# Kernel optimization log

Hardware: AMD Instinct MI355X
Metric: run time of the kernel (lower is better)

## Reference

```python
import jax, jax.numpy as jnp
import numpy as np
from jax import lax

IMG_H, IMG_W = 800.0, 800.0
REG_WEIGHTS = (10.0, 10.0, 5.0, 5.0)
SCORE_THRESH = 0.05
NMS_THRESH = 0.5
NUM_DETECTIONS = 100
MIN_SIZE = 1.0
BBOX_XFORM_CLIP = float(np.log(1000.0 / 16.0))


def setup_inputs() -> dict:
    key = jax.random.key(0)
    k1, k2, k3, k4 = jax.random.split(key, 4)
    N, C = 1000, 81
    class_logit = jax.random.normal(k1, (N, C), dtype=jnp.float32) * 2.0
    box_regression = jax.random.normal(k2, (N, C * 4), dtype=jnp.float32)
    # proposals: valid (x1,y1,x2,y2) boxes inside the 800x800 image
    ctr = jax.random.uniform(k3, (N, 2), dtype=jnp.float32) * 800.0
    wh = jax.random.uniform(k4, (N, 2), dtype=jnp.float32) * 200.0 + 8.0
    x1y1 = jnp.clip(ctr - 0.5 * wh, 0.0, 800.0)
    x2y2 = jnp.clip(ctr + 0.5 * wh, 0.0, 800.0)
    proposal = jnp.concatenate([x1y1, x2y2], axis=1)
    return dict(class_logit=class_logit, box_regression=box_regression, proposal=proposal)


def decode_boxes(deltas, boxes):
    # deltas: [..., 4] (dx,dy,dw,dh); boxes: [..., 4] (x1,y1,x2,y2)
    wx, wy, ww, wh = REG_WEIGHTS
    widths = boxes[..., 2] - boxes[..., 0]
    heights = boxes[..., 3] - boxes[..., 1]
    ctr_x = boxes[..., 0] + 0.5 * widths
    ctr_y = boxes[..., 1] + 0.5 * heights
    dx = deltas[..., 0] / wx
    dy = deltas[..., 1] / wy
    dw = jnp.minimum(deltas[..., 2] / ww, BBOX_XFORM_CLIP)
    dh = jnp.minimum(deltas[..., 3] / wh, BBOX_XFORM_CLIP)
    pcx = dx * widths + ctr_x
    pcy = dy * heights + ctr_y
    pw = jnp.exp(dw) * widths
    ph = jnp.exp(dh) * heights
    return jnp.stack([pcx - 0.5 * pw, pcy - 0.5 * ph, pcx + 0.5 * pw, pcy + 0.5 * ph], axis=-1)


def pairwise_iou(b):
    # b: [N, 4] -> [N, N]
    area = (b[:, 2] - b[:, 0]) * (b[:, 3] - b[:, 1])
    lt = jnp.maximum(b[:, None, :2], b[None, :, :2])
    rb = jnp.minimum(b[:, None, 2:], b[None, :, 2:])
    wh = jnp.clip(rb - lt, 0.0)
    inter = wh[..., 0] * wh[..., 1]
    return inter / (area[:, None] + area[None, :] - inter + 1e-9)


def nms_one_class(boxes, scores):
    # boxes: [N, 4]; scores: [N] with invalid entries masked to -1.
    # Exact greedy NMS: sort by score desc, suppress IoU > NMS_THRESH.
    N = boxes.shape[0]
    order = jnp.argsort(-scores)
    b = boxes[order]
    s = scores[order]
    iou = pairwise_iou(b)
    valid = s > -0.5

    def body(carry, xs):
        keep, i = carry
        row, v = xs
        suppressed = jnp.any(keep & (row > NMS_THRESH))
        keep = keep.at[i].set(v & jnp.logical_not(suppressed))
        return (keep, i + 1), None

    (keep, _), _ = lax.scan(body, (jnp.zeros((N,), bool), jnp.int32(0)), (iou, valid))
    s_kept = jnp.where(keep, s, -1.0)
    top_s, top_i = lax.top_k(s_kept, NUM_DETECTIONS)  # kept are already score-sorted
    out_valid = top_s > -0.5
    out_boxes = jnp.where(out_valid[:, None], b[top_i], 0.0)
    out_scores = jnp.where(out_valid, top_s, 0.0)
    return out_boxes, out_scores, out_valid


def reference(class_logit, box_regression, proposal):
    N, C = class_logit.shape
    pred_score = jax.nn.softmax(class_logit, axis=-1)           # [N, C]
    deltas = box_regression.reshape(N, C, 4)
    boxes = decode_boxes(deltas[:, 1:, :], proposal[:, None, :])  # [N, C-1, 4]
    # clip to image (process_box)
    boxes = jnp.stack([
        jnp.clip(boxes[..., 0], 0.0, IMG_W),
        jnp.clip(boxes[..., 1], 0.0, IMG_H),
        jnp.clip(boxes[..., 2], 0.0, IMG_W),
        jnp.clip(boxes[..., 3], 0.0, IMG_H),
    ], axis=-1)
    w = boxes[..., 2] - boxes[..., 0]
    h = boxes[..., 3] - boxes[..., 1]
    score_fg = pred_score[:, 1:]                                 # [N, C-1]
    valid = (score_fg >= SCORE_THRESH) & (w >= MIN_SIZE) & (h >= MIN_SIZE)
    scores_m = jnp.where(valid, score_fg, -1.0)
    boxes_c = jnp.transpose(boxes, (1, 0, 2))                    # [C-1, N, 4]
    scores_c = scores_m.T                                        # [C-1, N]
    out_boxes, out_scores, out_valid = jax.vmap(nms_one_class)(boxes_c, scores_c)
    labels = jnp.broadcast_to(jnp.arange(1, C, dtype=jnp.int32)[:, None], out_scores.shape)
    labels = jnp.where(out_valid, labels, 0)
    # padded per-class detections: boxes [C-1, D, 4], scores/labels/valid [C-1, D]
    return out_boxes, out_scores, labels, out_valid
```

## Files before the change

kernel.cpp:

```cpp
#include <hip/hip_runtime.h>
#include <math.h>

#define N_PROP   1000
#define C_ALL    81
#define N_FG     80
#define TOPK     100
#define CAP      1024
#define IMG_WH   800.0f
#define SCORE_TH 0.05f
#define NMS_TH   0.5f
#define MIN_SZ   1.0f
#define BBOX_CLIP 4.135166556742356f

typedef unsigned long long u64;

#define WS_REQUIRED (sizeof(float2) * N_PROP)

__global__ __launch_bounds__(256) void stats_kernel(
    const float* __restrict__ logits,
    float2* __restrict__ stats)
{
    const int wave = threadIdx.x >> 6;
    const int lane = threadIdx.x & 63;
    const int n = blockIdx.x * 4 + wave;
    if (n >= N_PROP) return;
    const float* row = logits + n * C_ALL;

    float v1 = row[lane];
    float v2 = (lane < C_ALL - 64) ? row[64 + lane] : 0.f;

    float m = (lane < C_ALL - 64) ? fmaxf(v1, v2) : v1;
    #pragma unroll
    for (int off = 32; off >= 1; off >>= 1)
        m = fmaxf(m, __shfl_xor(m, off, 64));

    float s = expf(v1 - m) + ((lane < C_ALL - 64) ? expf(v2 - m) : 0.0f);
    #pragma unroll
    for (int off = 32; off >= 1; off >>= 1)
        s += __shfl_xor(s, off, 64);

    if (lane == 0) stats[n] = make_float2(m, s);
}

__global__ __launch_bounds__(256) void nms_kernel(
    const float* __restrict__ logits,
    const float* __restrict__ boxreg,
    const float* __restrict__ prop,
    const float2* __restrict__ stats,
    float* __restrict__ out)
{
    __shared__ float2 s_ms[N_PROP];
    __shared__ unsigned short s_cn[CAP];
    __shared__ float s_csc[CAP];
    __shared__ u64   s_key[CAP];
    __shared__ float cx1[CAP], cy1[CAP], cx2[CAP], cy2[CAP], car[CAP];
    __shared__ u64   s_skey[CAP];
    __shared__ float sx1[CAP], sy1[CAP], sx2[CAP], sy2[CAP], sar[CAP];
    __shared__ u64   s_mask[256 * 4];
    __shared__ unsigned char s_rem[CAP];
    __shared__ unsigned short s_src[TOPK];
    __shared__ int   s_nc, s_cnt, s_emit, s_nk;

    const int c    = blockIdx.x;
    const int tid  = threadIdx.x;
    const int lane = tid & 63;
    const int col  = c + 1;

    const int OFF_SCORES = N_FG * TOPK * 4;
    const int OFF_LABELS = OFF_SCORES + N_FG * TOPK;
    const int OFF_VALID  = OFF_LABELS + N_FG * TOPK;

    if (tid == 0) { s_nc = 0; s_cnt = 0; s_emit = 0; s_nk = 0; }

    if (stats != nullptr) {
        for (int t = tid; t < N_PROP; t += 256) s_ms[t] = stats[t];
    } else {
        for (int n = tid; n < N_PROP; n += 256) {
            const float* row = logits + n * C_ALL;
            float m = -1e30f;
            for (int j = 0; j < C_ALL; ++j) m = fmaxf(m, row[j]);
            float s = 0.0f;
            for (int j = 0; j < C_ALL; ++j) s += expf(row[j] - m);
            s_ms[n] = make_float2(m, s);
        }
    }
    __syncthreads();

    #pragma unroll
    for (int k = 0; k < 4; ++k) {
        int n = k * 256 + tid;
        bool v = false; float sc = 0.0f;
        if (n < N_PROP) {
            float2 ms = s_ms[n];
            sc = expf(logits[n * C_ALL + col] - ms.x) / ms.y;
            v = (sc >= SCORE_TH);
        }
        u64 bal = __ballot(v);
        int pop = __popcll(bal);
        int wb = 0;
        if (lane == 0 && pop) wb = atomicAdd(&s_nc, pop);
        wb = __shfl(wb, 0, 64);
        if (v) {
            int slot = wb + __popcll(bal & ((1ull << lane) - 1ull));
            s_cn[slot]  = (unsigned short)n;
            s_csc[slot] = sc;
        }
    }
    __syncthreads();
    const int NC = s_nc;

    for (int t = tid; t < NC; t += 256) {
        int n = s_cn[t];
        float sc = s_csc[t];

        float4 p = *(const float4*)(prop + n * 4);
        float w  = p.z - p.x;
        float h  = p.w - p.y;
        float pcx0 = p.x + 0.5f * w;
        float pcy0 = p.y + 0.5f * h;

        float4 d = *(const float4*)(boxreg + n * (C_ALL * 4) + col * 4);
        float dx = d.x / 10.0f;
        float dy = d.y / 10.0f;
        float dw = fminf(d.z / 5.0f, BBOX_CLIP);
        float dh = fminf(d.w / 5.0f, BBOX_CLIP);

        float pcx = dx * w + pcx0;
        float pcy = dy * h + pcy0;
        float pw  = expf(dw) * w;
        float ph  = expf(dh) * h;

        float x1 = fminf(fmaxf(pcx - 0.5f * pw, 0.0f), IMG_WH);
        float y1 = fminf(fmaxf(pcy - 0.5f * ph, 0.0f), IMG_WH);
        float x2 = fminf(fmaxf(pcx + 0.5f * pw, 0.0f), IMG_WH);
        float y2 = fminf(fmaxf(pcy + 0.5f * ph, 0.0f), IMG_WH);

        float bw = x2 - x1;
        float bh = y2 - y1;
        if (bw >= MIN_SZ && bh >= MIN_SZ) {
            int slot = atomicAdd(&s_cnt, 1);
            s_key[slot] = ((u64)__float_as_uint(sc) << 10) | (u64)(1023 - n);
            cx1[slot] = x1; cy1[slot] = y1; cx2[slot] = x2; cy2[slot] = y2;
            car[slot] = bw * bh;
        }
    }
    __syncthreads();

    const int V = s_cnt;

    if (V > 0) {
        for (int t = tid; t < V; t += 256) {
            u64 myk = s_key[t];
            int rank = 0;
            #pragma unroll 4
            for (int j = 0; j < V; ++j) rank += (s_key[j] > myk) ? 1 : 0;
            s_skey[rank] = myk;
            sx1[rank] = cx1[t]; sy1[rank] = cy1[t];
            sx2[rank] = cx2[t]; sy2[rank] = cy2[t];
            sar[rank] = car[t];
        }
        __syncthreads();

        if (V <= 64) {
            if (tid < 64) {
                bool act = lane < V;
                float bx1 = 0.f, by1 = 0.f, bx2 = 0.f, by2 = 0.f, bar = 0.f;
                if (act) {
                    bx1 = sx1[lane]; by1 = sy1[lane];
                    bx2 = sx2[lane]; by2 = sy2[lane];
                    bar = sar[lane];
                }
                u64 myrow = 0;
                for (int i = 0; i < V; ++i) {
                    float ix1 = __shfl(bx1, i, 64);
                    float iy1 = __shfl(by1, i, 64);
                    float ix2 = __shfl(bx2, i, 64);
                    float iy2 = __shfl(by2, i, 64);
                    float iar = __shfl(bar, i, 64);
                    float lx = fmaxf(ix1, bx1);
                    float ly = fmaxf(iy1, by1);
                    float rx = fminf(ix2, bx2);
                    float ry = fminf(iy2, by2);
                    float iw = fmaxf(rx - lx, 0.0f);
                    float ih = fmaxf(ry - ly, 0.0f);
                    float inter = iw * ih;
                    float iou = inter / (iar + bar - inter + 1e-9f);
                    u64 bal = __ballot(act && (iou > NMS_TH));
                    if (lane == i) {
                        u64 upper = (i == 63) ? 0ull : ~((1ull << (i + 1)) - 1ull);
                        myrow = bal & upper;
                    }
                }
                u64 S = 0, K = 0;
                for (int i = 0; i < V; ++i) {
                    if (!((S >> i) & 1ull)) {
                        K |= 1ull << i;
                        S |= __shfl(myrow, i, 64);
                    }
                }
                if (act && ((K >> lane) & 1ull)) {
                    int rank = __popcll(K & ((1ull << lane) - 1ull));
                    s_src[rank] = (unsigned short)lane;
                }
                if (lane == 0) s_nk = __popcll(K);
            }
        } else if (V <= 256) {
            for (int i = tid; i < V; i += 256) {
                float x1i = sx1[i], y1i = sy1[i], x2i = sx2[i], y2i = sy2[i];
                float ai  = sar[i];
                for (int w = 0; w < 4; ++w) {
                    u64 mrow = 0;
                    int j0 = w << 6;
                    int j1 = min(V, j0 + 64);
                    for (int j = max(j0, i + 1); j < j1; ++j) {
                        float lx = fmaxf(x1i, sx1[j]);
                        float ly = fmaxf(y1i, sy1[j]);
                        float rx = fminf(x2i, sx2[j]);
                        float ry = fminf(y2i, sy2[j]);
                        float iw = fmaxf(rx - lx, 0.0f);
                        float ih = fmaxf(ry - ly, 0.0f);
                        float inter = iw * ih;
                        float iou = inter / (ai + sar[j] - inter + 1e-9f);
                        if (iou > NMS_TH) mrow |= 1ull << (j - j0);
                    }
                    s_mask[(i << 2) + w] = mrow;
                }
            }
            __syncthreads();

            if (tid == 0) {
                u64 r0 = 0, r1 = 0, r2 = 0, r3 = 0;
                int kept = 0;
                u64 p0 = s_mask[0], p1 = s_mask[1], p2 = s_mask[2], p3 = s_mask[3];
                u64 q0 = 0, q1 = 0, q2 = 0, q3 = 0;
                if (V > 1) {
                    const u64* nr = &s_mask[4];
                    q0 = nr[0]; q1 = nr[1]; q2 = nr[2]; q3 = nr[3];
                }
                for (int i = 0; i < V; ++i) {
                    u64 t0 = 0, t1 = 0, t2 = 0, t3 = 0;
                    if (i + 2 < V) {
                        const u64* nr = &s_mask[(i + 2) << 2];
                        t0 = nr[0]; t1 = nr[1]; t2 = nr[2]; t3 = nr[3];
                    }
                    int w = i >> 6;
                    u64 bit = 1ull << (i & 63);
                    u64 rw = (w == 0) ? r0 : (w == 1) ? r1 : (w == 2) ? r2 : r3;
                    if (!(rw & bit)) {
                        s_src[kept] = (unsigned short)i;
                        if (++kept >= TOPK) break;
                        r0 |= p0; r1 |= p1; r2 |= p2; r3 |= p3;
                    }
                    p0 = q0; p1 = q1; p2 = q2; p3 = q3;
                    q0 = t0; q1 = t1; q2 = t2; q3 = t3;
                }
                s_nk = kept;
            }
        } else {
            for (int t = tid; t < V; t += 256) s_rem[t] = 0;
            __syncthreads();
            for (int i = 0; i < V; ++i) {
                if (s_rem[i]) continue;
                if (tid == 0) {
                    int k = s_emit;
                    if (k < TOPK) s_src[k] = (unsigned short)i;
                    s_emit = k + 1;
                }
                float x1i = sx1[i], y1i = sy1[i], x2i = sx2[i], y2i = sy2[i];
                float ai  = sar[i];
                for (int jj = i + 1 + tid; jj < V; jj += 256) {
                    if (s_rem[jj]) continue;
                    float lx = fmaxf(x1i, sx1[jj]);
                    float ly = fmaxf(y1i, sy1[jj]);
                    float rx = fminf(x2i, sx2[jj]);
                    float ry = fminf(y2i, sy2[jj]);
                    float iw = fmaxf(rx - lx, 0.0f);
                    float ih = fmaxf(ry - ly, 0.0f);
                    float inter = iw * ih;
                    float iou = inter / (ai + sar[jj] - inter + 1e-9f);
                    if (iou > NMS_TH) s_rem[jj] = 1;
                }
                __syncthreads();
                if (s_emit >= TOPK) break;
            }
            if (tid == 0) s_nk = min(s_emit, TOPK);
        }
    }
    __syncthreads();

    const int nk = s_nk;
    if (tid < TOPK) {
        float4 bx = make_float4(0.f, 0.f, 0.f, 0.f);
        float sc = 0.f, lb = 0.f, vd = 0.f;
        if (tid < nk) {
            int s = s_src[tid];
            bx = make_float4(sx1[s], sy1[s], sx2[s], sy2[s]);
            sc = __uint_as_float((unsigned int)(s_skey[s] >> 10));
            lb = (float)col;
            vd = 1.0f;
        }
        ((float4*)out)[c * TOPK + tid] = bx;
        out[OFF_SCORES + c * TOPK + tid] = sc;
        out[OFF_LABELS + c * TOPK + tid] = lb;
        out[OFF_VALID  + c * TOPK + tid] = vd;
    }
}

extern "C" void kernel_launch(void* const* d_in, const int* in_sizes, int n_in,
                              void* d_out, int out_size, void* d_ws, size_t ws_size,
                              hipStream_t stream) {
    const float* class_logit = (const float*)d_in[0];
    const float* box_reg     = (const float*)d_in[1];
    const float* proposal    = (const float*)d_in[2];
    float* out = (float*)d_out;

    float2* stats = (ws_size >= WS_REQUIRED) ? (float2*)d_ws : nullptr;

    if (stats) {
        stats_kernel<<<(N_PROP + 3) / 4, 256, 0, stream>>>(class_logit, stats);
    }
    nms_kernel<<<N_FG, 256, 0, stream>>>(class_logit, box_reg, proposal,
                                         stats, out);
}
```

Measured before the change: 83.62 us.

## Widen NMS block to 512 threads and parallelize mask rows across words

Raises the NMS block size to 512 threads. Per-proposal stats are now read straight from global memory instead of being staged into shared memory, and each thread handles two proposals in the score filter. The IoU mask build for V<=256 now assigns a (row, 64-column word) pair to each thread, which cuts the serial inner loop per thread. The dedicated single-wave path for V<=64 is removed, so small candidate sets fall back to the general mask path. This adds shared-memory traffic and a block-wide barrier for those small cases.

Result: no change. 82.88 us (-0.9%).

```diff
diff --git a/kernel.cpp b/kernel.cpp
--- a/kernel.cpp
+++ b/kernel.cpp
@@ -12,6 +12,8 @@
 #define MIN_SZ   1.0f
 #define BBOX_CLIP 4.135166556742356f
 
+#define NMS_BLK  512
+
 typedef unsigned long long u64;
 
 #define WS_REQUIRED (sizeof(float2) * N_PROP)
@@ -42,7 +44,7 @@
     if (lane == 0) stats[n] = make_float2(m, s);
 }
 
-__global__ __launch_bounds__(256) void nms_kernel(
+__global__ __launch_bounds__(NMS_BLK) void nms_kernel(
     const float* __restrict__ logits,
     const float* __restrict__ boxreg,
     const float* __restrict__ prop,
@@ -72,10 +74,8 @@
 
     if (tid == 0) { s_nc = 0; s_cnt = 0; s_emit = 0; s_nk = 0; }
 
-    if (stats != nullptr) {
-        for (int t = tid; t < N_PROP; t += 256) s_ms[t] = stats[t];
-    } else {
-        for (int n = tid; n < N_PROP; n += 256) {
+    if (stats == nullptr) {
+        for (int n = tid; n < N_PROP; n += NMS_BLK) {
             const float* row = logits + n * C_ALL;
             float m = -1e30f;
             for (int j = 0; j < C_ALL; ++j) m = fmaxf(m, row[j]);
@@ -86,30 +86,48 @@
     }
     __syncthreads();
 
-    #pragma unroll
-    for (int k = 0; k < 4; ++k) {
-        int n = k * 256 + tid;
-        bool v = false; float sc = 0.0f;
-        if (n < N_PROP) {
-            float2 ms = s_ms[n];
-            sc = expf(logits[n * C_ALL + col] - ms.x) / ms.y;
-            v = (sc >= SCORE_TH);
-        }
-        u64 bal = __ballot(v);
+    {
+        const int n0 = tid;
+        const int n1 = NMS_BLK + tid;
+        const bool has1 = (n1 < N_PROP);
+
+        float  l0 = logits[n0 * C_ALL + col];
+        float2 m0 = stats ? stats[n0] : s_ms[n0];
+        float  l1 = 0.0f;
+        float2 m1 = make_float2(0.f, 1.f);
+        if (has1) { l1 = logits[n1 * C_ALL + col]; m1 = stats ? stats[n1] : s_ms[n1]; }
+
+        float sc0 = expf(l0 - m0.x) / m0.y;
+        float sc1 = has1 ? (expf(l1 - m1.x) / m1.y) : 0.0f;
+
+        bool v0 = (sc0 >= SCORE_TH);
+        u64 bal = __ballot(v0);
         int pop = __popcll(bal);
         int wb = 0;
         if (lane == 0 && pop) wb = atomicAdd(&s_nc, pop);
         wb = __shfl(wb, 0, 64);
-        if (v) {
+        if (v0) {
             int slot = wb + __popcll(bal & ((1ull << lane) - 1ull));
-            s_cn[slot]  = (unsigned short)n;
-            s_csc[slot] = sc;
+            s_cn[slot]  = (unsigned short)n0;
+            s_csc[slot] = sc0;
+        }
+
+        bool v1 = has1 && (sc1 >= SCORE_TH);
+        bal = __ballot(v1);
+        pop = __popcll(bal);
+        wb = 0;
+        if (lane == 0 && pop) wb = atomicAdd(&s_nc, pop);
+        wb = __shfl(wb, 0, 64);
+        if (v1) {
+            int slot = wb + __popcll(bal & ((1ull << lane) - 1ull));
+            s_cn[slot]  = (unsigned short)n1;
+            s_csc[slot] = sc1;
         }
     }
     __syncthreads();
     const int NC = s_nc;
 
-    for (int t = tid; t < NC; t += 256) {
+    for (int t = tid; t < NC; t += NMS_BLK) {
         int n = s_cn[t];
         float sc = s_csc[t];
 
@@ -149,7 +167,7 @@
     const int V = s_cnt;
 
     if (V > 0) {
-        for (int t = tid; t < V; t += 256) {
+        for (int t = tid; t < V; t += NMS_BLK) {
             u64 myk = s_key[t];
             int rank = 0;
             #pragma unroll 4
@@ -161,54 +179,14 @@
         }
         __syncthreads();
 
-        if (V <= 64) {
-            if (tid < 64) {
-                bool act = lane < V;
-                float bx1 = 0.f, by1 = 0.f, bx2 = 0.f, by2 = 0.f, bar = 0.f;
-                if (act) {
-                    bx1 = sx1[lane]; by1 = sy1[lane];
-                    bx2 = sx2[lane]; by2 = sy2[lane];
-                    bar = sar[lane];
-                }
-                u64 myrow = 0;
-                for (int i = 0; i < V; ++i) {
-                    float ix1 = __shfl(bx1, i, 64);
-                    float iy1 = __shfl(by1, i, 64);
-                    float ix2 = __shfl(bx2, i, 64);
-                    float iy2 = __shfl(by2, i, 64);
-                    float iar = __shfl(bar, i, 64);
-                    float lx = fmaxf(ix1, bx1);
-                    float ly = fmaxf(iy1, by1);
-                    float rx = fminf(ix2, bx2);
-                    float ry = fminf(iy2, by2);
-                    float iw = fmaxf(rx - lx, 0.0f);
-                    float ih = fmaxf(ry - ly, 0.0f);
-                    float inter = iw * ih;
-                    float iou = inter / (iar + bar - inter + 1e-9f);
-                    u64 bal = __ballot(act && (iou > NMS_TH));
-                    if (lane == i) {
-                        u64 upper = (i == 63) ? 0ull : ~((1ull << (i + 1)) - 1ull);
-                        myrow = bal & upper;
-                    }
-                }
-                u64 S = 0, K = 0;
-                for (int i = 0; i < V; ++i) {
-                    if (!((S >> i) & 1ull)) {
-                        K |= 1ull << i;
-                        S |= __shfl(myrow, i, 64);
-                    }
-                }
-                if (act && ((K >> lane) & 1ull)) {
-                    int rank = __popcll(K & ((1ull << lane) - 1ull));
-                    s_src[rank] = (unsigned short)lane;
-                }
-                if (lane == 0) s_nk = __popcll(K);
-            }
-        } else if (V <= 256) {
-            for (int i = tid; i < V; i += 256) {
-                float x1i = sx1[i], y1i = sy1[i], x2i = sx2[i], y2i = sy2[i];
-                float ai  = sar[i];
-                for (int w = 0; w < 4; ++w) {
+        if (V <= 256) {
+            for (int i0 = 0; i0 < V; i0 += 128) {
+                int i = i0 + (tid & 127);
+                int w = tid >> 7;
+                if (i < V) {
+                    float x1i = sx1[i], y1i = sy1[i];
+                    float x2i = sx2[i], y2i = sy2[i];
+                    float ai  = sar[i];
                     u64 mrow = 0;
                     int j0 = w << 6;
                     int j1 = min(V, j0 + 64);
@@ -257,7 +235,7 @@
                 s_nk = kept;
             }
         } else {
-            for (int t = tid; t < V; t += 256) s_rem[t] = 0;
+            for (int t = tid; t < V; t += NMS_BLK) s_rem[t] = 0;
             __syncthreads();
             for (int i = 0; i < V; ++i) {
                 if (s_rem[i]) continue;
@@ -268,7 +246,7 @@
                 }
                 float x1i = sx1[i], y1i = sy1[i], x2i = sx2[i], y2i = sy2[i];
                 float ai  = sar[i];
-                for (int jj = i + 1 + tid; jj < V; jj += 256) {
+                for (int jj = i + 1 + tid; jj < V; jj += NMS_BLK) {
                     if (s_rem[jj]) continue;
                     float lx = fmaxf(x1i, sx1[jj]);
                     float ly = fmaxf(y1i, sy1[jj]);
@@ -319,6 +297,6 @@
     if (stats) {
         stats_kernel<<<(N_PROP + 3) / 4, 256, 0, stream>>>(class_logit, stats);
     }
-    nms_kernel<<<N_FG, 256, 0, stream>>>(class_logit, box_reg, proposal,
-                                         stats, out);
+    nms_kernel<<<N_FG, NMS_BLK, 0, stream>>>(class_logit, box_reg, proposal,
+                                             stats, out);
 }
```
